# Optimization experiments

Hardware: AMD Instinct MI355X
Metric: run time of the kernel (lower is better)

The kernel has to match this reference:

```python
import jax, jax.numpy as jnp
import numpy as np

B, H, W, C = 1, 256, 256, 256  # pooled feature map, NHWC
OH, OW = 2 * H, 2 * W          # unpooled output spatial dims


def setup_inputs() -> dict:
    key = jax.random.key(0)
    val = jax.random.normal(key, (B, H, W, C), dtype=jnp.float32)
    # Canonical argmax indices: each pooled element maps to the top-left
    # corner of its 2x2 window in the flattened [OH, OW, C] output.
    h = jnp.arange(H, dtype=jnp.int32)[:, None, None]   # [H,1,1]
    w = jnp.arange(W, dtype=jnp.int32)[None, :, None]   # [1,W,1]
    c = jnp.arange(C, dtype=jnp.int32)[None, None, :]   # [1,1,C]
    index = ((2 * h) * OW + (2 * w)) * C + c            # [H,W,C]
    index = jnp.broadcast_to(index, (B, H, W, C))
    return {"val": val, "index": index}


def reference(val, index):
    # tf.scatter_nd into a flat buffer of size OH*OW*C (duplicates sum),
    # then reshape to [-1, OH, OW, C].
    flat = jnp.zeros((OH * OW * C,), dtype=val.dtype)
    flat = flat.at[index.reshape(-1)].add(val.reshape(-1))
    return flat.reshape(-1, OH, OW, C)
```

## Files before the change

kernel.cpp:

```cpp
#include <hip/hip_runtime.h>


typedef float  f32x4 __attribute__((ext_vector_type(4)));
typedef int    i32x4 __attribute__((ext_vector_type(4)));

__global__ __launch_bounds__(256) void unpool_oc4_kernel(
    const float* __restrict__ val,
    const int*   __restrict__ idx,
    float*       __restrict__ out)
{
    constexpr int G   = 1 << 22;
    constexpr int GIN = 1 << 20;

    const int tid = blockIdx.x * blockDim.x + threadIdx.x;

    f32x4* o = reinterpret_cast<f32x4*>(out);
    const f32x4 z = (f32x4)(0.f);

    const int c4  = tid & 63;
    const int ow  = (tid >> 6) & 511;
    const int oh0 = tid >> 15;

    if ((oh0 | ow) & 1) {
        #pragma unroll
        for (int k = 0; k < 4; ++k)
            o[tid + k * G] = z;
        return;
    }

    const int qin0 = ((oh0 >> 1) << 14) + ((ow >> 1) << 6) + c4;
    const f32x4* vq = reinterpret_cast<const f32x4*>(val);
    const i32x4* iq = reinterpret_cast<const i32x4*>(idx);

    f32x4 v[4];
    i32x4 id[4];
    #pragma unroll
    for (int k = 0; k < 4; ++k) {
        v[k]  = __builtin_nontemporal_load(vq + qin0 + k * GIN);
        id[k] = __builtin_nontemporal_load(iq + qin0 + k * GIN);
    }

    #pragma unroll
    for (int k = 0; k < 4; ++k) {
        const int q = tid + k * G;
        const int p = q << 2;
        if (__builtin_expect(id[k].x == p     && id[k].y == p + 1 &&
                             id[k].z == p + 2 && id[k].w == p + 3, 1)) {
            o[q] = v[k];
        } else {
            o[q] = z;
            atomicAdd(out + id[k].x, v[k].x);
            atomicAdd(out + id[k].y, v[k].y);
            atomicAdd(out + id[k].z, v[k].z);
            atomicAdd(out + id[k].w, v[k].w);
        }
    }
}

extern "C" void kernel_launch(void* const* d_in, const int* in_sizes, int n_in,
                              void* d_out, int out_size, void* d_ws, size_t ws_size,
                              hipStream_t stream) {
    const float* val = (const float*)d_in[0];
    const int*   idx = (const int*)d_in[1];
    float* out = (float*)d_out;

    const int n       = in_sizes[0];
    const int threads = n / 4;
    const int block   = 256;
    const int grid    = threads / block;
    unpool_oc4_kernel<<<grid, block, 0, stream>>>(val, idx, out);
}
```

Measured before the change: 356.8 us.

## Remap threads so each wave writes a contiguous row segment of output

Reassigns work so each 64-lane wave covers eight consecutive output pixels in a row and reads four consecutive input pixels. This replaces the old scheme, where each thread wrote four widely separated quarters of the output. Odd rows and odd columns are zero-filled inside the same contiguous span. The aim is better DRAM locality for writes and reads, at the cost of fewer independent loads in flight per thread on odd rows.

```diff
diff --git a/kernel.cpp b/kernel.cpp
--- a/kernel.cpp
+++ b/kernel.cpp
@@ -4,45 +4,50 @@
 typedef float  f32x4 __attribute__((ext_vector_type(4)));
 typedef int    i32x4 __attribute__((ext_vector_type(4)));
 
-__global__ __launch_bounds__(256) void unpool_oc4_kernel(
+__global__ __launch_bounds__(256) void unpool_wc8_kernel(
     const float* __restrict__ val,
     const int*   __restrict__ idx,
     float*       __restrict__ out)
 {
-    constexpr int G   = 1 << 22;
-    constexpr int GIN = 1 << 20;
+    const int t    = blockIdx.x * blockDim.x + threadIdx.x;
+    const int lane = t & 63;
+    const int wid  = t >> 6;
 
-    const int tid = blockIdx.x * blockDim.x + threadIdx.x;
+    const int baseq = wid << 9;
+    const int pix0  = wid << 3;
+    const int oh    = pix0 >> 9;
 
     f32x4* o = reinterpret_cast<f32x4*>(out);
     const f32x4 z = (f32x4)(0.f);
 
-    const int c4  = tid & 63;
-    const int ow  = (tid >> 6) & 511;
-    const int oh0 = tid >> 15;
-
-    if ((oh0 | ow) & 1) {
+    if (oh & 1) {
         #pragma unroll
-        for (int k = 0; k < 4; ++k)
-            o[tid + k * G] = z;
+        for (int i = 0; i < 8; ++i)
+            o[baseq + i * 64 + lane] = z;
         return;
     }
 
-    const int qin0 = ((oh0 >> 1) << 14) + ((ow >> 1) << 6) + c4;
+    const int h    = oh >> 1;
+    const int w0   = (pix0 & 511) >> 1;
+    const int qin0 = (h << 14) + (w0 << 6) + lane;
+
     const f32x4* vq = reinterpret_cast<const f32x4*>(val);
     const i32x4* iq = reinterpret_cast<const i32x4*>(idx);
 
-    f32x4 v[4];
-    i32x4 id[4];
+    f32x4 v[4]; i32x4 id[4];
     #pragma unroll
     for (int k = 0; k < 4; ++k) {
-        v[k]  = __builtin_nontemporal_load(vq + qin0 + k * GIN);
-        id[k] = __builtin_nontemporal_load(iq + qin0 + k * GIN);
+        v[k]  = __builtin_nontemporal_load(vq + qin0 + k * 64);
+        id[k] = __builtin_nontemporal_load(iq + qin0 + k * 64);
     }
 
     #pragma unroll
+    for (int k = 0; k < 4; ++k)
+        o[baseq + (2 * k + 1) * 64 + lane] = z;
+
+    #pragma unroll
     for (int k = 0; k < 4; ++k) {
-        const int q = tid + k * G;
+        const int q = baseq + 2 * k * 64 + lane;
         const int p = q << 2;
         if (__builtin_expect(id[k].x == p     && id[k].y == p + 1 &&
                              id[k].z == p + 2 && id[k].w == p + 3, 1)) {
@@ -65,8 +70,8 @@
     float* out = (float*)d_out;
 
     const int n       = in_sizes[0];
-    const int threads = n / 4;
+    const int threads = n / 8;
     const int block   = 256;
     const int grid    = threads / block;
-    unpool_oc4_kernel<<<grid, block, 0, stream>>>(val, idx, out);
+    unpool_wc8_kernel<<<grid, block, 0, stream>>>(val, idx, out);
 }
```

Result: faster. 345.9 us (-3.1%).
